# Kernel optimization log

Hardware: AMD Instinct MI355X
Metric: run time of the kernel (lower is better)

Reference implementation:

```python
import jax, jax.numpy as jnp
import numpy as np

B, S, E, H = 2, 2048, 2048, 16
D = E // H  # head_dim = 128


def rotate_half(x):
    x1, x2 = jnp.split(x, 2, axis=-1)
    return jnp.concatenate([-x2, x1], axis=-1)


def rope_sincos(seq_len, dim):
    inv_freq = 1.0 / (10000.0 ** (jnp.arange(0, dim, 2, dtype=jnp.float32) / dim))
    t = jnp.arange(seq_len, dtype=jnp.float32)
    freqs = jnp.outer(t, inv_freq)            # [S, D/2]
    emb = jnp.concatenate([freqs, freqs], -1)  # [S, D]
    return jnp.sin(emb), jnp.cos(emb)


def apply_rope(x, sin, cos):
    # x: [B, S, H, D]; sin/cos: [S, D] -> [1, S, 1, D]
    sin = sin[None, :, None, :]
    cos = cos[None, :, None, :]
    return x * cos + rotate_half(x) * sin


def setup_inputs() -> dict:
    key = jax.random.key(0)
    k1, k2 = jax.random.split(key)
    x = jax.random.normal(k1, (B, S, E), dtype=jnp.float32)
    # causal boolean mask [B, 1, S, S]
    mask = jnp.broadcast_to(jnp.tril(jnp.ones((S, S), dtype=bool))[None, None], (B, 1, S, S))
    # fused QKV projection weight (hk.Linear, no bias): [E, 3E]
    W_qkv = jax.random.normal(k2, (E, 3 * E), dtype=jnp.float32) / np.sqrt(E)
    return {"x": x, "mask": mask, "W_qkv": W_qkv}


def reference(x, mask, W_qkv):
    seq_len = x.shape[1]
    qkv = x @ W_qkv                               # [B, S, 3E]
    q, k, v = jnp.split(qkv, 3, axis=-1)
    q = q.reshape(-1, seq_len, H, D)
    k = k.reshape(-1, seq_len, H, D)
    v = v.reshape(-1, seq_len, H, D)
    sin, cos = rope_sincos(seq_len, D)
    q = apply_rope(q, sin, cos)
    k = apply_rope(k, sin, cos)
    attn = jnp.einsum('bqhd,bkhd->bhqk', q, k) / jnp.sqrt(jnp.float32(D))
    m = jnp.broadcast_to(mask, (mask.shape[0], H, seq_len, k.shape[1]))
    attn = jnp.where(m, attn, -jnp.inf)
    attn = jax.nn.softmax(attn, axis=-1)
    out = jnp.einsum('bhqk,bkhd->bqhd', attn, v)
    return out.reshape(-1, seq_len, H * D)
```

## Files before the change

### kernel.cpp

```cpp
#include <hip/hip_runtime.h>

typedef __bf16 bf16;
typedef __bf16 bf16x8 __attribute__((ext_vector_type(8)));
typedef __bf16 bf16x4 __attribute__((ext_vector_type(4)));
typedef float f32x4 __attribute__((ext_vector_type(4)));

#define MFMA16(a, b, c) __builtin_amdgcn_mfma_f32_16x16x32_bf16(a, b, c, 0, 0, 0)

#define Bq 2
#define Sq 2048
#define Eq 2048
#define Hq 16
#define Dq 128
#define N3E 6144

#define GLOAD_LDS16(gp, lp) \
  __builtin_amdgcn_global_load_lds( \
      (const __attribute__((address_space(1))) void*)(gp), \
      (__attribute__((address_space(3))) void*)(lp), 16, 0, 0)

__device__ __forceinline__ bf16 f2bf(float f) {
  unsigned u = __builtin_bit_cast(unsigned, f);
  u += 0x7FFFu + ((u >> 16) & 1u);
  unsigned short h = (unsigned short)(u >> 16);
  return __builtin_bit_cast(bf16, h);
}
__device__ __forceinline__ float bf2f(bf16 b) {
  unsigned short h = __builtin_bit_cast(unsigned short, b);
  return __builtin_bit_cast(float, (unsigned)h << 16);
}

__global__ __launch_bounds__(256) void prep(const float* __restrict__ x,
                                            bf16* __restrict__ xb,
                                            const float* __restrict__ w,
                                            bf16* __restrict__ wt,
                                            float2* __restrict__ tbl) {
  __shared__ __align__(16) bf16 T[64][72];
  const int tid = threadIdx.x;
  const int bidx = blockIdx.x;

  if (bidx < 4096) {
    const size_t i = ((size_t)bidx * 256 + tid) * 8;
    float4 a = *(const float4*)(x + i);
    float4 b = *(const float4*)(x + i + 4);
    bf16x8 o;
    o[0] = f2bf(a.x); o[1] = f2bf(a.y); o[2] = f2bf(a.z); o[3] = f2bf(a.w);
    o[4] = f2bf(b.x); o[5] = f2bf(b.y); o[6] = f2bf(b.z); o[7] = f2bf(b.w);
    *(bf16x8*)(xb + i) = o;
  } else if (bidx < 4096 + 3072) {
    const int b2 = bidx - 4096;
    const int kb = b2 & 31;
    const int nb = b2 >> 5;
    const int k0 = kb * 64, n0 = nb * 64;
    {
      const int kr = tid >> 4, nc = (tid & 15) * 4;
#pragma unroll
      for (int p = 0; p < 4; ++p) {
        const int k = kr + p * 16;
        float4 v = *(const float4*)(w + (size_t)(k0 + k) * N3E + n0 + nc);
        T[nc + 0][k] = f2bf(v.x);
        T[nc + 1][k] = f2bf(v.y);
        T[nc + 2][k] = f2bf(v.z);
        T[nc + 3][k] = f2bf(v.w);
      }
    }
    __syncthreads();
#pragma unroll
    for (int q = 0; q < 2; ++q) {
      const int id = q * 256 + tid;
      const int n = id >> 3, ch = id & 7;
      bf16x8 v = *(const bf16x8*)&T[n][ch * 8];
      *(bf16x8*)(wt + (size_t)(n0 + n) * Eq + k0 + ch * 8) = v;
    }
  } else {
    const int i = (bidx - 7168) * 256 + tid;
    const int s = i >> 6, d = i & 63;
    const float freq = __expf(-(float)d * 0.14391157f);
    const float ang = (float)s * freq;
    float sv, cv;
    __sincosf(ang, &sv, &cv);
    tbl[i] = make_float2(cv, sv);
  }
}

__global__ __launch_bounds__(512, 2) void gemm_qkv(
    const bf16* __restrict__ xb, const bf16* __restrict__ wt,
    const float2* __restrict__ tbl, bf16* __restrict__ qws,
    bf16* __restrict__ kws, bf16* __restrict__ vtws) {
  __shared__ __align__(16) bf16 LDS[3 * 24576];

  const int tid = threadIdx.x;
  const int lane = tid & 63, wv = tid >> 6;
  const int q4 = lane >> 4, c = lane & 15;
  const int wm = (wv >> 2) * 64;
  const int wn = (wv & 3) * 64;
  const int cx = c & 7;

  const int bid = blockIdx.x;
  const int wg = (bid & 7) * 96 + (bid >> 3);
  const int m0 = (wg / 24) * 128;
  const int n0 = (wg % 24) * 256;

  f32x4 acc[4][4];
#pragma unroll
  for (int i = 0; i < 4; ++i)
#pragma unroll
    for (int j = 0; j < 4; ++j) acc[i][j] = {0.f, 0.f, 0.f, 0.f};

  const int NT = Eq / 64;

  auto stage = [&](int t, int st) {
    bf16* ab = LDS + st * 24576;
    bf16* bb = ab + 8192;
    const int k0 = t * 64;
#pragma unroll
    for (int it = 0; it < 2; ++it) {
      const int slot = it * 512 + tid;
      const int row = slot >> 3, kch = slot & 7;
      const int kcs = kch ^ (row & 7);
      GLOAD_LDS16(xb + (size_t)(m0 + row) * Eq + k0 + kcs * 8, ab + slot * 8);
    }
#pragma unroll
    for (int it = 0; it < 4; ++it) {
      const int slot = it * 512 + tid;
      const int row = slot >> 3, kch = slot & 7;
      const int kcs = kch ^ (row & 7);
      GLOAD_LDS16(wt + (size_t)(n0 + row) * Eq + k0 + kcs * 8, bb + slot * 8);
    }
  };

  stage(0, 0);
  stage(1, 1);
  asm volatile("s_waitcnt vmcnt(6)" ::: "memory");
  __builtin_amdgcn_s_barrier();

  int stC = 0;
#pragma unroll 1
  for (int t = 0; t < NT; ++t) {
    if (t + 2 < NT) {
      int ss = stC + 2;
      if (ss >= 3) ss -= 3;
      stage(t + 2, ss);
    }
    const bf16* A = LDS + stC * 24576;
    const bf16* Bb = A + 8192;
#pragma unroll
    for (int kk = 0; kk < 64; kk += 32) {
      const int bch = kk >> 3;
      bf16x8 af[4], bfr[4];
#pragma unroll
      for (int i = 0; i < 4; ++i)
        af[i] = *(const bf16x8*)
            &A[(wm + i * 16 + c) * 64 + ((bch + q4) ^ cx) * 8];
#pragma unroll
      for (int j = 0; j < 4; ++j)
        bfr[j] = *(const bf16x8*)
            &Bb[(wn + j * 16 + c) * 64 + ((bch + q4) ^ cx) * 8];
      __builtin_amdgcn_s_setprio(1);
#pragma unroll
      for (int i = 0; i < 4; ++i)
#pragma unroll
        for (int j = 0; j < 4; ++j)
          acc[i][j] = MFMA16(af[i], bfr[j], acc[i][j]);
      __builtin_amdgcn_s_setprio(0);
    }
    if (t + 1 < NT) {
      if (t + 2 < NT) asm volatile("s_waitcnt vmcnt(6)" ::: "memory");
      else            asm volatile("s_waitcnt vmcnt(0)" ::: "memory");
      __builtin_amdgcn_s_barrier();
    }
    stC = stC == 2 ? 0 : stC + 1;
  }
  __syncthreads();

  const int t3 = n0 >> 11;
  const int b = m0 >> 11;
  const int s0 = m0 & 2047;
  const int h0 = (n0 & 2047) >> 7;

  bf16* E = LDS;

  if (t3 == 2) {
#pragma unroll 1
    for (int hh = 0; hh < 2; ++hh) {
      if (((wv & 3) >> 1) == hh) {
#pragma unroll
        for (int i = 0; i < 4; ++i)
#pragma unroll
          for (int j = 0; j < 4; ++j) {
            bf16x4 pv;
            pv[0] = f2bf(acc[i][j][0]); pv[1] = f2bf(acc[i][j][1]);
            pv[2] = f2bf(acc[i][j][2]); pv[3] = f2bf(acc[i][j][3]);
            *(bf16x4*)&E[((wn & 127) + j * 16 + c) * 136 + wm + i * 16 +
                         q4 * 4] = pv;
          }
      }
      __syncthreads();
      bf16* vbase = vtws + ((size_t)(b * Hq + h0 + hh) * Dq) * Sq + s0;
#pragma unroll
      for (int p = 0; p < 4; ++p) {
        const int id = p * 512 + tid;
        const int d = id >> 4, ch = id & 15;
        bf16x8 v = *(const bf16x8*)&E[d * 136 + ch * 8];
        *(bf16x8*)&vbase[(size_t)d * Sq + ch * 8] = v;
      }
      __syncthreads();
    }
  } else {
#pragma unroll 1
    for (int hh = 0; hh < 2; ++hh) {
      if (((wv & 3) >> 1) == hh) {
#pragma unroll
        for (int i = 0; i < 4; ++i)
#pragma unroll
          for (int j = 0; j < 4; ++j)
#pragma unroll
            for (int rr = 0; rr < 4; ++rr)
              E[(wm + i * 16 + q4 * 4 + rr) * 136 + (wn & 127) + j * 16 + c] =
                  f2bf(acc[i][j][rr]);
      }
      __syncthreads();
      bf16* hd = ((t3 == 0) ? qws : kws) +
                 ((size_t)(b * Hq + h0 + hh) * Sq + s0) * Dq;
#pragma unroll
      for (int p = 0; p < 2; ++p) {
        const int row = p * 64 + (tid >> 3);
        const int dlow = (tid & 7) * 8;
        const int s = s0 + row;
        bf16x8 lo = *(const bf16x8*)&E[row * 136 + dlow];
        bf16x8 hi = *(const bf16x8*)&E[row * 136 + 64 + dlow];
        const float2* tb = tbl + (size_t)s * 64 + dlow;
        bf16x8 olo, ohi;
#pragma unroll
        for (int e = 0; e < 8; ++e) {
          const float cv = tb[e].x, sv = tb[e].y;
          const float x1 = bf2f(lo[e]), x2 = bf2f(hi[e]);
          olo[e] = f2bf(x1 * cv - x2 * sv);
          ohi[e] = f2bf(x2 * cv + x1 * sv);
        }
        *(bf16x8*)&hd[(size_t)row * Dq + dlow] = olo;
        *(bf16x8*)&hd[(size_t)row * Dq + 64 + dlow] = ohi;
      }
      __syncthreads();
    }
  }
}

__global__ __launch_bounds__(256, 2) void attn_kernel(
    const bf16* __restrict__ qws, const bf16* __restrict__ kws,
    const bf16* __restrict__ vtws, float* __restrict__ out) {
  __shared__ __align__(16) bf16 Kld[2][8192];
  __shared__ __align__(16) bf16 Vld[2][8192];
  __shared__ __align__(16) bf16 Plds[4][16][72];

  const int tid = threadIdx.x, lane = tid & 63, wave = tid >> 6;
  const int q4 = lane >> 4, c = lane & 15;
  const int h = blockIdx.y, b = blockIdx.z;
  const int qt = b ? blockIdx.x : (15 - blockIdx.x);
  const size_t bh = (size_t)(b * Hq + h);
  const bf16* qbase = qws + bh * Sq * Dq;
  const bf16* kbase = kws + bh * Sq * Dq;
  const bf16* vbase = vtws + bh * Dq * Sq;
  const int q0 = qt * 128 + wave * 32;
  const float kSc = 0.08838834764831845f * 1.4426950408889634f;

  bf16x8 qf[2][4];
#pragma unroll
  for (int g = 0; g < 2; ++g)
#pragma unroll
    for (int ks = 0; ks < 4; ++ks)
      qf[g][ks] = *(const bf16x8*)
          &qbase[(size_t)(q0 + g * 16 + c) * Dq + ks * 32 + q4 * 8];

  f32x4 Ot[2][8];
  float m_i[2], l_i[2];
#pragma unroll
  for (int g = 0; g < 2; ++g) {
#pragma unroll
    for (int dj = 0; dj < 8; ++dj) Ot[g][dj] = {0.f, 0.f, 0.f, 0.f};
    m_i[g] = -1e30f; l_i[g] = 0.f;
  }

  const int nchunks = 2 * qt + 2;

#pragma unroll
  for (int it = 0; it < 4; ++it) {
    const int slot = it * 256 + tid;
    GLOAD_LDS16(kbase + (size_t)(slot & 63) * Dq + (slot >> 6) * 8,
                &Kld[0][slot * 8]);
    GLOAD_LDS16(vbase + (size_t)(slot & 127) * Sq + (slot >> 7) * 8,
                &Vld[0][slot * 8]);
  }
  __syncthreads();

  for (int kb = 0; kb < nchunks; ++kb) {
    const int buf = kb & 1;
    if (kb + 1 < nchunks) {
      const int nb = buf ^ 1;
      const int koff = (kb + 1) * 64;
#pragma unroll
      for (int it = 0; it < 4; ++it) {
        const int slot = it * 256 + tid;
        GLOAD_LDS16(kbase + (size_t)(koff + (slot & 63)) * Dq + (slot >> 6) * 8,
                    &Kld[nb][slot * 8]);
        GLOAD_LDS16(vbase + (size_t)(slot & 127) * Sq + koff + (slot >> 7) * 8,
                    &Vld[nb][slot * 8]);
      }
    }
    const bool masked = (kb >= 2 * qt);
#pragma unroll
    for (int g = 0; g < 2; ++g) {
      const int qg = q0 + g * 16 + c;
      f32x4 st[4];
#pragma unroll
      for (int j8 = 0; j8 < 4; ++j8) st[j8] = {0.f, 0.f, 0.f, 0.f};
      __builtin_amdgcn_s_setprio(1);
#pragma unroll
      for (int ks = 0; ks < 4; ++ks) {
        const bf16x8 qv = qf[g][ks];
#pragma unroll
        for (int j8 = 0; j8 < 4; ++j8) {
          const bf16x8 kv = *(const bf16x8*)
              &Kld[buf][((ks * 4 + q4) * 64 + j8 * 16 + c) * 8];
          st[j8] = MFMA16(kv, qv, st[j8]);
        }
      }
      __builtin_amdgcn_s_setprio(0);
      if (masked) {
        const int kb64 = kb * 64 + q4 * 4;
#pragma unroll
        for (int j8 = 0; j8 < 4; ++j8)
#pragma unroll
          for (int rr = 0; rr < 4; ++rr)
            if (kb64 + j8 * 16 + rr > qg) st[j8][rr] = -1e30f;
      }
      float mloc = -1e30f;
#pragma unroll
      for (int j8 = 0; j8 < 4; ++j8)
#pragma unroll
        for (int rr = 0; rr < 4; ++rr) mloc = fmaxf(mloc, st[j8][rr]);
      mloc = fmaxf(mloc, __shfl_xor(mloc, 16, 64));
      mloc = fmaxf(mloc, __shfl_xor(mloc, 32, 64));
      float mn = m_i[g];
      if (__any(mloc > mn)) {
        mn = fmaxf(mn, mloc);
        const float alpha = exp2f((m_i[g] - mn) * kSc);
        m_i[g] = mn;
        l_i[g] *= alpha;
#pragma unroll
        for (int dj = 0; dj < 8; ++dj) Ot[g][dj] *= alpha;
      }
      float ssum = 0.f;
#pragma unroll
      for (int j8 = 0; j8 < 4; ++j8)
#pragma unroll
        for (int rr = 0; rr < 4; ++rr) {
          const float p = exp2f((st[j8][rr] - mn) * kSc);
          st[j8][rr] = p;
          ssum += p;
        }
      ssum += __shfl_xor(ssum, 16, 64);
      ssum += __shfl_xor(ssum, 32, 64);
      l_i[g] += ssum;
#pragma unroll
      for (int j8 = 0; j8 < 4; ++j8) {
        bf16x4 pk;
        pk[0] = f2bf(st[j8][0]); pk[1] = f2bf(st[j8][1]);
        pk[2] = f2bf(st[j8][2]); pk[3] = f2bf(st[j8][3]);
        *(bf16x4*)&Plds[wave][c][j8 * 16 + q4 * 4] = pk;
      }
      __builtin_amdgcn_s_setprio(1);
#pragma unroll
      for (int ks = 0; ks < 2; ++ks) {
        const bf16x8 pv = *(const bf16x8*)&Plds[wave][c][ks * 32 + q4 * 8];
#pragma unroll
        for (int dj = 0; dj < 8; ++dj) {
          const bf16x8 vv = *(const bf16x8*)
              &Vld[buf][((ks * 4 + q4) * 128 + dj * 16 + c) * 8];
          Ot[g][dj] = MFMA16(vv, pv, Ot[g][dj]);
        }
      }
      __builtin_amdgcn_s_setprio(0);
    }
    __syncthreads();
  }

#pragma unroll
  for (int g = 0; g < 2; ++g) {
    const float inv = 1.0f / l_i[g];
    float* orow = out + ((size_t)b * Sq + q0 + g * 16 + c) * Eq + h * Dq;
#pragma unroll
    for (int dj = 0; dj < 8; ++dj) {
      float4 o;
      o.x = Ot[g][dj][0] * inv; o.y = Ot[g][dj][1] * inv;
      o.z = Ot[g][dj][2] * inv; o.w = Ot[g][dj][3] * inv;
      *(float4*)&orow[dj * 16 + q4 * 4] = o;
    }
  }
}

extern "C" void kernel_launch(void* const* d_in, const int* in_sizes, int n_in,
                              void* d_out, int out_size, void* d_ws,
                              size_t ws_size, hipStream_t stream) {
  const float* x = (const float*)d_in[0];
  const float* w = (const float*)d_in[2];
  float* out = (float*)d_out;

  const size_t nX = (size_t)Bq * Sq * Eq;
  const size_t nW = (size_t)Eq * N3E;
  const size_t perT = (size_t)Bq * Hq * Sq * Dq;

  bf16* xb = (bf16*)d_ws;
  bf16* wt = xb + nX;
  bf16* qws = wt + nW;
  bf16* kws = qws + perT;
  bf16* vtws = kws + perT;
  float2* tbl = (float2*)(vtws + perT);

  prep<<<7680, 256, 0, stream>>>(x, xb, w, wt, tbl);

  gemm_qkv<<<768, 512, 0, stream>>>(xb, wt, tbl, qws, kws, vtws);

  dim3 g3(Sq / 128, Hq, Bq);
  attn_kernel<<<g3, 256, 0, stream>>>(qws, kws, vtws, out);
}
```

Measured before the change: 374.8 us.

## Split long causal query tiles across two blocks and merge with a combine kernel

The causal attention kernel now splits the eight longest query tiles per (batch, head) into two blocks. Each block handles half of the key chunks and writes unnormalized partial outputs plus running max and sum to workspace. A new combine kernel merges each pair with log-sum-exp weights. This is meant to even out per-block work and shorten the tail of the grid, at the cost of extra fp32 partial-output traffic and one more launch. The partial buffers reuse the start of the workspace, which is presumably safe because xb and wt are no longer needed once the QKV GEMM has finished.

```diff
diff --git a/kernel.cpp b/kernel.cpp
--- a/kernel.cpp
+++ b/kernel.cpp
@@ -246,9 +246,12 @@
   }
 }
 
+#define KSC (0.08838834764831845f * 1.4426950408889634f)
+
 __global__ __launch_bounds__(256, 2) void attn_kernel(
     const bf16* __restrict__ qws, const bf16* __restrict__ kws,
-    const bf16* __restrict__ vtws, float* __restrict__ out) {
+    const bf16* __restrict__ vtws, float* __restrict__ out,
+    float* __restrict__ opart, float* __restrict__ ml) {
   __shared__ __align__(16) bf16 Kld[2][8192];
   __shared__ __align__(16) bf16 Vld[2][8192];
   __shared__ __align__(16) bf16 Plds[4][16][72];
@@ -256,13 +259,29 @@
   const int tid = threadIdx.x, lane = tid & 63, wave = tid >> 6;
   const int q4 = lane >> 4, c = lane & 15;
   const int h = blockIdx.y, b = blockIdx.z;
-  const int qt = b ? blockIdx.x : (15 - blockIdx.x);
+
+  const int xid = blockIdx.x;
+  int qt, c0, c1, sp;
+  bool split;
+  if (xid < 16) {
+    split = true;
+    qt = 15 - (xid >> 1);
+    sp = xid & 1;
+    c0 = sp * (qt + 1);
+    c1 = c0 + (qt + 1);
+  } else {
+    split = false;
+    qt = 23 - xid;
+    sp = 0;
+    c0 = 0;
+    c1 = 2 * qt + 2;
+  }
+
   const size_t bh = (size_t)(b * Hq + h);
   const bf16* qbase = qws + bh * Sq * Dq;
   const bf16* kbase = kws + bh * Sq * Dq;
   const bf16* vbase = vtws + bh * Dq * Sq;
   const int q0 = qt * 128 + wave * 32;
-  const float kSc = 0.08838834764831845f * 1.4426950408889634f;
 
   bf16x8 qf[2][4];
 #pragma unroll
@@ -281,21 +300,22 @@
     m_i[g] = -1e30f; l_i[g] = 0.f;
   }
 
-  const int nchunks = 2 * qt + 2;
-
-#pragma unroll
-  for (int it = 0; it < 4; ++it) {
-    const int slot = it * 256 + tid;
-    GLOAD_LDS16(kbase + (size_t)(slot & 63) * Dq + (slot >> 6) * 8,
-                &Kld[0][slot * 8]);
-    GLOAD_LDS16(vbase + (size_t)(slot & 127) * Sq + (slot >> 7) * 8,
-                &Vld[0][slot * 8]);
+  {
+    const int koff0 = c0 * 64;
+#pragma unroll
+    for (int it = 0; it < 4; ++it) {
+      const int slot = it * 256 + tid;
+      GLOAD_LDS16(kbase + (size_t)(koff0 + (slot & 63)) * Dq + (slot >> 6) * 8,
+                  &Kld[c0 & 1][slot * 8]);
+      GLOAD_LDS16(vbase + (size_t)(slot & 127) * Sq + koff0 + (slot >> 7) * 8,
+                  &Vld[c0 & 1][slot * 8]);
+    }
   }
   __syncthreads();
 
-  for (int kb = 0; kb < nchunks; ++kb) {
+  for (int kb = c0; kb < c1; ++kb) {
     const int buf = kb & 1;
-    if (kb + 1 < nchunks) {
+    if (kb + 1 < c1) {
       const int nb = buf ^ 1;
       const int koff = (kb + 1) * 64;
 #pragma unroll
@@ -344,7 +364,7 @@
       float mn = m_i[g];
       if (__any(mloc > mn)) {
         mn = fmaxf(mn, mloc);
-        const float alpha = exp2f((m_i[g] - mn) * kSc);
+        const float alpha = exp2f((m_i[g] - mn) * KSC);
         m_i[g] = mn;
         l_i[g] *= alpha;
 #pragma unroll
@@ -355,7 +375,7 @@
       for (int j8 = 0; j8 < 4; ++j8)
 #pragma unroll
         for (int rr = 0; rr < 4; ++rr) {
-          const float p = exp2f((st[j8][rr] - mn) * kSc);
+          const float p = exp2f((st[j8][rr] - mn) * KSC);
           st[j8][rr] = p;
           ssum += p;
         }
@@ -385,17 +405,75 @@
     __syncthreads();
   }
 
-#pragma unroll
-  for (int g = 0; g < 2; ++g) {
-    const float inv = 1.0f / l_i[g];
-    float* orow = out + ((size_t)b * Sq + q0 + g * 16 + c) * Eq + h * Dq;
-#pragma unroll
-    for (int dj = 0; dj < 8; ++dj) {
-      float4 o;
-      o.x = Ot[g][dj][0] * inv; o.y = Ot[g][dj][1] * inv;
-      o.z = Ot[g][dj][2] * inv; o.w = Ot[g][dj][3] * inv;
-      *(float4*)&orow[dj * 16 + q4 * 4] = o;
-    }
+  if (!split) {
+#pragma unroll
+    for (int g = 0; g < 2; ++g) {
+      const float inv = 1.0f / l_i[g];
+      float* orow = out + ((size_t)b * Sq + q0 + g * 16 + c) * Eq + h * Dq;
+#pragma unroll
+      for (int dj = 0; dj < 8; ++dj) {
+        float4 o;
+        o.x = Ot[g][dj][0] * inv; o.y = Ot[g][dj][1] * inv;
+        o.z = Ot[g][dj][2] * inv; o.w = Ot[g][dj][3] * inv;
+        *(float4*)&orow[dj * 16 + q4 * 4] = o;
+      }
+    }
+  } else {
+    const int tix = (((b * Hq + h) * 8) + (qt - 8)) * 2 + sp;
+#pragma unroll
+    for (int g = 0; g < 2; ++g) {
+      const int wrow = wave * 32 + g * 16 + c;
+      float* prow = opart + ((size_t)tix * 128 + wrow) * 128;
+#pragma unroll
+      for (int dj = 0; dj < 8; ++dj) {
+        float4 o;
+        o.x = Ot[g][dj][0]; o.y = Ot[g][dj][1];
+        o.z = Ot[g][dj][2]; o.w = Ot[g][dj][3];
+        *(float4*)&prow[dj * 16 + q4 * 4] = o;
+      }
+      if (q4 == 0) {
+        ml[((size_t)tix * 128 + wrow) * 2 + 0] = m_i[g];
+        ml[((size_t)tix * 128 + wrow) * 2 + 1] = l_i[g];
+      }
+    }
+  }
+}
+
+__global__ __launch_bounds__(256) void attn_combine(
+    const float* __restrict__ opart, const float* __restrict__ ml,
+    float* __restrict__ out) {
+  const int tile = blockIdx.x;
+  const int qt = (tile & 7) + 8;
+  const int hb = tile >> 3;
+  const int h = hb & 15, b = hb >> 4;
+  const int tid = threadIdx.x;
+  const int r = tid >> 1;
+  const int d0 = (tid & 1) * 64;
+  const int t0 = tile * 2, t1 = t0 + 1;
+
+  const float m0 = ml[((size_t)t0 * 128 + r) * 2 + 0];
+  const float l0 = ml[((size_t)t0 * 128 + r) * 2 + 1];
+  const float m1 = ml[((size_t)t1 * 128 + r) * 2 + 0];
+  const float l1 = ml[((size_t)t1 * 128 + r) * 2 + 1];
+  const float m = fmaxf(m0, m1);
+  const float w0 = exp2f((m0 - m) * KSC);
+  const float w1 = exp2f((m1 - m) * KSC);
+  const float inv = 1.0f / (l0 * w0 + l1 * w1);
+  const float s0 = w0 * inv, s1 = w1 * inv;
+
+  const float* p0 = opart + ((size_t)t0 * 128 + r) * 128 + d0;
+  const float* p1 = opart + ((size_t)t1 * 128 + r) * 128 + d0;
+  float* orow = out + ((size_t)(b * Sq + qt * 128 + r)) * Eq + h * Dq + d0;
+#pragma unroll
+  for (int i = 0; i < 16; ++i) {
+    float4 a = *(const float4*)&p0[i * 4];
+    float4 bb = *(const float4*)&p1[i * 4];
+    float4 o;
+    o.x = a.x * s0 + bb.x * s1;
+    o.y = a.y * s0 + bb.y * s1;
+    o.z = a.z * s0 + bb.z * s1;
+    o.w = a.w * s0 + bb.w * s1;
+    *(float4*)&orow[i * 4] = o;
   }
 }
 
@@ -417,10 +495,15 @@
   bf16* vtws = kws + perT;
   float2* tbl = (float2*)(vtws + perT);
 
+  float* opart = (float*)d_ws;
+  float* ml = opart + (size_t)512 * 128 * 128;
+
   prep<<<7680, 256, 0, stream>>>(x, xb, w, wt, tbl);
 
   gemm_qkv<<<768, 512, 0, stream>>>(xb, wt, tbl, qws, kws, vtws);
 
-  dim3 g3(Sq / 128, Hq, Bq);
-  attn_kernel<<<g3, 256, 0, stream>>>(qws, kws, vtws, out);
-}
+  dim3 g3(24, 16, 2);
+  attn_kernel<<<g3, 256, 0, stream>>>(qws, kws, vtws, out, opart, ml);
+
+  attn_combine<<<256, 256, 0, stream>>>(opart, ml, out);
+}
```

Result: slower. 396.7 us (+5.8%).
